# Kernel optimization log

Hardware: AMD Instinct MI355X
Metric: run time of the kernel (lower is better)

Reference implementation:

```python
import jax, jax.numpy as jnp
import numpy as np

N, E, IN, H, OUT, G = 40000, 640000, 128, 128, 16, 64


def _sage(x, src, dst, Wl, Wr, b, n):
    # PyG SAGEConv (aggr='mean'): out = lin_l(mean_j x_j) + lin_r(x_i); bias in lin_l only
    msg = jnp.take(x, src, axis=0)                      # [E, d] gather
    s = jax.ops.segment_sum(msg, dst, num_segments=n)   # [N, d] scatter-add
    cnt = jax.ops.segment_sum(jnp.ones((src.shape[0], 1), x.dtype), dst, num_segments=n)
    agg = s / jnp.maximum(cnt, 1.0)                     # mean; 0 for isolated nodes
    return agg @ Wl.T + x @ Wr.T + b


def setup_inputs() -> dict:
    key = jax.random.key(0)
    ks = jax.random.split(key, 12)
    x = jax.random.normal(ks[0], (N, IN), jnp.float32)
    edge_index = jax.random.randint(ks[1], (2, E), 0, N, jnp.int64)
    batch = jnp.sort(jax.random.randint(ks[2], (N,), 0, G, jnp.int64))
    def lin(k, o, i):
        return jax.random.normal(k, (o, i), jnp.float32) / np.sqrt(i)
    return {
        "x": x, "edge_index": edge_index, "batch": batch,
        "W1l": lin(ks[3], H, IN), "W1r": lin(ks[4], H, IN), "b1": jnp.zeros((H,), jnp.float32),
        "W2l": lin(ks[5], H, H),  "W2r": lin(ks[6], H, H),  "b2": jnp.zeros((H,), jnp.float32),
        "W3l": lin(ks[7], H, H),  "W3r": lin(ks[8], H, H),  "b3": jnp.zeros((H,), jnp.float32),
        "Wfc": lin(ks[9], OUT, H), "bfc": jnp.zeros((OUT,), jnp.float32),
    }


def reference(x, edge_index, batch, W1l, W1r, b1, W2l, W2r, b2, W3l, W3r, b3, Wfc, bfc):
    src, dst = edge_index[0], edge_index[1]
    n = x.shape[0]
    h = jax.nn.relu(_sage(x, src, dst, W1l, W1r, b1, n))
    h = jax.nn.relu(_sage(h, src, dst, W2l, W2r, b2, n))
    h = jax.nn.relu(_sage(h, src, dst, W3l, W3r, b3, n))
    # global_mean_pool over graph ids
    s = jax.ops.segment_sum(h, batch, num_segments=G)
    cnt = jax.ops.segment_sum(jnp.ones((n, 1), h.dtype), batch, num_segments=G)
    pooled = s / jnp.maximum(cnt, 1.0)                  # [G, H]
    return pooled @ Wfc.T + bfc                          # [G, OUT]
```

## Files before the change

### kernel.cpp

```cpp
#include <hip/hip_runtime.h>

static constexpr int D = 128;
static constexpr int PS = 32;

typedef __attribute__((ext_vector_type(8))) short short8;
typedef __attribute__((ext_vector_type(4))) float f32x4;

__device__ inline ushort f2bf(float f) {
  union { float f; unsigned u; } v; v.f = f;
  unsigned r = v.u + 0x7FFF + ((v.u >> 16) & 1);
  return (ushort)(r >> 16);
}
__device__ inline float bf2f_lo(unsigned p) {
  union { unsigned u; float f; } v; v.u = p << 16; return v.f;
}
__device__ inline float bf2f_hi(unsigned p) {
  union { unsigned u; float f; } v; v.u = p & 0xFFFF0000u; return v.f;
}

struct WPtrs { const float* s[6]; ushort* d[6]; };

__global__ __launch_bounds__(256) void k_prep(const float* __restrict__ x, ushort* __restrict__ xb, WPtrs p,
                                              const int* __restrict__ dst, int* __restrict__ hist,
                                              int n4x, int E) {
  int b = blockIdx.x, tid = threadIdx.x;
  int nxb = (n4x + 255) / 256;
  if (b < nxb) {
    int i = b * 256 + tid;
    if (i < n4x) {
      float4 v = *(const float4*)&x[i * 4];
      ushort4 o;
      o.x = f2bf(v.x); o.y = f2bf(v.y); o.z = f2bf(v.z); o.w = f2bf(v.w);
      *(ushort4*)&xb[i * 4] = o;
    }
  } else if (b < nxb + 96) {
    int idx = (b - nxb) * 256 + tid;
    int mat = idx >> 12;
    int off = (idx & 4095) * 4;
    float4 v = *(const float4*)&p.s[mat][off];
    ushort4 o;
    o.x = f2bf(v.x); o.y = f2bf(v.y); o.z = f2bf(v.z); o.w = f2bf(v.w);
    *(ushort4*)&p.d[mat][off] = o;
  } else {
    int e = (b - nxb - 96) * 256 + tid;
    if (e < E) atomicAdd(&hist[dst[e]], 1);
  }
}

__global__ __launch_bounds__(1024) void k_scan(const int* __restrict__ hist, int* __restrict__ offsets, int n) {
  __shared__ int wsum[16];
  int tid = threadIdx.x, lane = tid & 63, w = tid >> 6;
  int carry = 0;
  for (int base = 0; base < n; base += 8192) {
    int i0 = base + tid * 8;
    int v[8];
    #pragma unroll
    for (int j = 0; j < 8; ++j) { int i = i0 + j; v[j] = (i < n) ? hist[i] : 0; }
    int s = 0;
    #pragma unroll
    for (int j = 0; j < 8; ++j) { int t = v[j]; v[j] = s; s += t; }
    int x = s;
    #pragma unroll
    for (int off = 1; off < 64; off <<= 1) {
      int t = __shfl_up(x, off);
      if (lane >= off) x += t;
    }
    if (lane == 63) wsum[w] = x;
    __syncthreads();
    int wpre = 0, total = 0;
    #pragma unroll
    for (int k = 0; k < 16; ++k) { int t = wsum[k]; total += t; if (k < w) wpre += t; }
    int pre = carry + wpre + x - s;
    #pragma unroll
    for (int j = 0; j < 8; ++j) { int i = i0 + j; if (i < n) offsets[i] = pre + v[j]; }
    carry += total;
    __syncthreads();
  }
  if (tid == 0) offsets[n] = carry;
}

__global__ __launch_bounds__(256) void k_fill(const int* __restrict__ src, const int* __restrict__ dst,
                                              const int* __restrict__ offsets, int* __restrict__ cursor,
                                              int* __restrict__ ssrc, int E) {
  int e = blockIdx.x * 256 + threadIdx.x;
  if (e < E) {
    int d = dst[e];
    int pos = offsets[d] + atomicAdd(&cursor[d], 1);
    ssrc[pos] = src[e];
  }
}

__global__ __launch_bounds__(256) void k_layer(const ushort* __restrict__ Xin,
                                               const int* __restrict__ offsets, const int* __restrict__ ssrc,
                                               const ushort* __restrict__ Wl, const ushort* __restrict__ Wr,
                                               const float* __restrict__ bias, ushort* __restrict__ Out, int n) {
  __shared__ ushort atile[64][136];
  int tid = threadIdx.x;
  int wave = tid >> 6, lane = tid & 63;
  int q = lane >> 4, r = lane & 15;
  int base = blockIdx.x * 64;

  for (int i = 0; i < 16; ++i) {
    int node = base + wave * 16 + i;
    float acc[8];
    #pragma unroll
    for (int t = 0; t < 8; ++t) acc[t] = 0.f;
    int deg = 0;
    if (node < n) {
      int o0 = offsets[node];
      deg = offsets[node + 1] - o0;
      for (int c0 = 0; c0 < deg; c0 += 64) {
        int cn = min(64, deg - c0);
        int myid = (lane < cn) ? ssrc[o0 + c0 + lane] : 0;
        for (int j = 0; j < cn; j += 16) {
          uint4 buf[4];
          #pragma unroll
          for (int t = 0; t < 4; ++t) {
            int e = j + t * 4 + q;
            buf[t] = (uint4){0u, 0u, 0u, 0u};
            if (e < cn) {
              int s = __shfl(myid, e);
              buf[t] = *(const uint4*)&Xin[(size_t)s * D + r * 8];
            }
          }
          #pragma unroll
          for (int t = 0; t < 4; ++t) {
            acc[0] += bf2f_lo(buf[t].x); acc[1] += bf2f_hi(buf[t].x);
            acc[2] += bf2f_lo(buf[t].y); acc[3] += bf2f_hi(buf[t].y);
            acc[4] += bf2f_lo(buf[t].z); acc[5] += bf2f_hi(buf[t].z);
            acc[6] += bf2f_lo(buf[t].w); acc[7] += bf2f_hi(buf[t].w);
          }
        }
      }
    }
    #pragma unroll
    for (int t = 0; t < 8; ++t) {
      acc[t] += __shfl_xor(acc[t], 16);
      acc[t] += __shfl_xor(acc[t], 32);
    }
    if (q == 0) {
      float inv = 1.f / (float)max(deg, 1);
      uint4 o;
      o.x = (unsigned)f2bf(acc[0] * inv) | ((unsigned)f2bf(acc[1] * inv) << 16);
      o.y = (unsigned)f2bf(acc[2] * inv) | ((unsigned)f2bf(acc[3] * inv) << 16);
      o.z = (unsigned)f2bf(acc[4] * inv) | ((unsigned)f2bf(acc[5] * inv) << 16);
      o.w = (unsigned)f2bf(acc[6] * inv) | ((unsigned)f2bf(acc[7] * inv) << 16);
      *(uint4*)&atile[wave * 16 + i][r * 8] = o;
    }
  }
  __syncthreads();

  int wm = wave >> 1, wn = wave & 1;
  int m_base = base + wm * 32;
  int n_base = wn * 64;
  int kg = lane >> 4;

  f32x4 acc[2][4];
  #pragma unroll
  for (int i = 0; i < 2; ++i)
    #pragma unroll
    for (int j = 0; j < 4; ++j) acc[i][j] = (f32x4){0.f, 0.f, 0.f, 0.f};

  #pragma unroll
  for (int k0 = 0; k0 < 128; k0 += 32) {
    int kk = k0 + kg * 8;
    short8 a0[2], a1[2], b0[4], b1[4];
    #pragma unroll
    for (int fm = 0; fm < 2; ++fm) {
      a0[fm] = *(const short8*)&atile[wm * 32 + fm * 16 + r][kk];
      a1[fm] = *(const short8*)&Xin[(size_t)(m_base + fm * 16 + r) * D + kk];
    }
    #pragma unroll
    for (int fn = 0; fn < 4; ++fn) {
      b0[fn] = *(const short8*)&Wl[(size_t)(n_base + fn * 16 + r) * D + kk];
      b1[fn] = *(const short8*)&Wr[(size_t)(n_base + fn * 16 + r) * D + kk];
    }
    #pragma unroll
    for (int fm = 0; fm < 2; ++fm)
      #pragma unroll
      for (int fn = 0; fn < 4; ++fn) {
        acc[fm][fn] = __builtin_amdgcn_mfma_f32_16x16x32_bf16(a0[fm], b0[fn], acc[fm][fn], 0, 0, 0);
        acc[fm][fn] = __builtin_amdgcn_mfma_f32_16x16x32_bf16(a1[fm], b1[fn], acc[fm][fn], 0, 0, 0);
      }
  }
  #pragma unroll
  for (int fn = 0; fn < 4; ++fn) {
    int j = n_base + fn * 16 + r;
    float bj = bias[j];
    #pragma unroll
    for (int fm = 0; fm < 2; ++fm) {
      #pragma unroll
      for (int p = 0; p < 4; ++p) {
        int node = m_base + fm * 16 + kg * 4 + p;
        if (node < n) {
          float v = fmaxf(acc[fm][fn][p] + bj, 0.f);
          Out[(size_t)node * D + j] = f2bf(v);
        }
      }
    }
  }
}

__global__ __launch_bounds__(256) void k_pool_partial(const ushort* __restrict__ H, const int* __restrict__ batch,
                                                      float* __restrict__ partial, int n) {
  __shared__ float wsums[4][128];
  int g = blockIdx.x / PS, s = blockIdx.x % PS;
  int tid = threadIdx.x, wave = tid >> 6, lane = tid & 63;
  int a = 0, b = n;
  while (a < b) { int m = (a + b) >> 1; if (batch[m] < g) a = m + 1; else b = m; }
  int lo = a;
  b = n;
  while (a < b) { int m = (a + b) >> 1; if (batch[m] < g + 1) a = m + 1; else b = m; }
  int hi = a;
  int len = hi - lo;
  int chunk = (len + PS - 1) / PS;
  int a0 = lo + s * chunk;
  int a1 = min(a0 + chunk, hi);
  float ax = 0.f, ay = 0.f;
  for (int node = a0 + wave; node < a1; node += 4) {
    unsigned v = *(const unsigned*)&H[(size_t)node * D + lane * 2];
    ax += bf2f_lo(v);
    ay += bf2f_hi(v);
  }
  wsums[wave][lane * 2] = ax;
  wsums[wave][lane * 2 + 1] = ay;
  __syncthreads();
  if (tid < 128) {
    float v = wsums[0][tid] + wsums[1][tid] + wsums[2][tid] + wsums[3][tid];
    partial[(size_t)blockIdx.x * 128 + tid] = v;
  }
}

__global__ __launch_bounds__(256) void k_pool_fc2(const float* __restrict__ partial, const int* __restrict__ batch,
                                                  const float* __restrict__ Wfc, const float* __restrict__ bfc,
                                                  float* __restrict__ out, int n, int OUT) {
  __shared__ float pooled[128];
  int g = blockIdx.x;
  int tid = threadIdx.x, lane = tid & 63;
  int a = 0, b = n;
  while (a < b) { int m = (a + b) >> 1; if (batch[m] < g) a = m + 1; else b = m; }
  int lo = a;
  b = n;
  while (a < b) { int m = (a + b) >> 1; if (batch[m] < g + 1) a = m + 1; else b = m; }
  int hi = a;
  float inv = 1.f / (float)max(hi - lo, 1);
  if (tid < 128) {
    float v = 0.f;
    #pragma unroll
    for (int s = 0; s < PS; ++s) v += partial[(size_t)(g * PS + s) * 128 + tid];
    pooled[tid] = v * inv;
  }
  __syncthreads();
  if (tid < 64) {
    float2 p = *(const float2*)&pooled[lane * 2];
    for (int o = 0; o < OUT; ++o) {
      float2 w = *(const float2*)&Wfc[o * D + lane * 2];
      float part = p.x * w.x + p.y * w.y;
      #pragma unroll
      for (int off = 32; off > 0; off >>= 1) part += __shfl_down(part, off);
      if (lane == 0) out[g * OUT + o] = part + bfc[o];
    }
  }
}

extern "C" void kernel_launch(void* const* d_in, const int* in_sizes, int n_in,
                              void* d_out, int out_size, void* d_ws, size_t ws_size,
                              hipStream_t stream) {
  const float* x   = (const float*)d_in[0];
  const int* ei    = (const int*)d_in[1];
  const int* batch = (const int*)d_in[2];
  const float* W1l = (const float*)d_in[3];
  const float* W1r = (const float*)d_in[4];
  const float* b1  = (const float*)d_in[5];
  const float* W2l = (const float*)d_in[6];
  const float* W2r = (const float*)d_in[7];
  const float* b2  = (const float*)d_in[8];
  const float* W3l = (const float*)d_in[9];
  const float* W3r = (const float*)d_in[10];
  const float* b3  = (const float*)d_in[11];
  const float* Wfc = (const float*)d_in[12];
  const float* bfc = (const float*)d_in[13];
  float* out = (float*)d_out;

  int N = in_sizes[0] / D;
  int E = in_sizes[1] / 2;
  int OUT = in_sizes[12] / D;
  int G = out_size / OUT;
  const int* src = ei;
  const int* dst = ei + E;

  ushort* xb  = (ushort*)d_ws;
  ushort* h1  = xb + (size_t)N * D;
  ushort* h2  = h1 + (size_t)N * D;
  ushort* wb  = h2 + (size_t)N * D;
  int* ssrc   = (int*)(wb + 6 * 128 * 128);
  int* hist   = ssrc + E;
  int* cursor = hist + N;
  int* offsets = cursor + N;
  float* partial = (float*)(offsets + N + 2);

  ushort* wl1 = wb + 0 * 16384; ushort* wr1 = wb + 1 * 16384;
  ushort* wl2 = wb + 2 * 16384; ushort* wr2 = wb + 3 * 16384;
  ushort* wl3 = wb + 4 * 16384; ushort* wr3 = wb + 5 * 16384;

  hipMemsetAsync(hist, 0, (size_t)2 * N * 4, stream);

  WPtrs wp;
  wp.s[0] = W1l; wp.s[1] = W1r; wp.s[2] = W2l; wp.s[3] = W2r; wp.s[4] = W3l; wp.s[5] = W3r;
  wp.d[0] = wl1; wp.d[1] = wr1; wp.d[2] = wl2; wp.d[3] = wr2; wp.d[4] = wl3; wp.d[5] = wr3;

  int n4 = N * D / 4;
  int nxb = (n4 + 255) / 256;
  int eb = (E + 255) / 256;
  k_prep<<<nxb + 96 + eb, 256, 0, stream>>>(x, xb, wp, dst, hist, n4, E);
  k_scan<<<1, 1024, 0, stream>>>(hist, offsets, N);
  k_fill<<<eb, 256, 0, stream>>>(src, dst, offsets, cursor, ssrc, E);

  int gb = (N + 63) / 64;
  k_layer<<<gb, 256, 0, stream>>>(xb, offsets, ssrc, wl1, wr1, b1, h1, N);
  k_layer<<<gb, 256, 0, stream>>>(h1, offsets, ssrc, wl2, wr2, b2, h2, N);
  k_layer<<<gb, 256, 0, stream>>>(h2, offsets, ssrc, wl3, wr3, b3, h1, N);

  k_pool_partial<<<G * PS, 256, 0, stream>>>(h1, batch, partial, N);
  k_pool_fc2<<<G, 256, 0, stream>>>(partial, batch, Wfc, bfc, out, N, OUT);
}
```

Measured before the change: 321.3 us.

## Shrink layer tile to 16 nodes per block and replace memset with zero kernel

The fused SAGE layer kernel now handles 16 nodes per block instead of 64. Each wave aggregates 4 nodes and then computes a 16x32 output slice with MFMA, running the Wl pass and the Wr pass back to back. This gives four times as many blocks, spreading the irregular gather work more evenly across CUs and cutting per-block serial aggregation length, at the cost of more redundant weight loads per output. The hipMemsetAsync that cleared the histogram is replaced by a small zeroing kernel, meant to avoid memset launch overhead.

```diff
diff --git a/kernel.cpp b/kernel.cpp
--- a/kernel.cpp
+++ b/kernel.cpp
@@ -19,6 +19,11 @@
 }
 
 struct WPtrs { const float* s[6]; ushort* d[6]; };
+
+__global__ __launch_bounds__(256) void k_zero(uint4* __restrict__ p, int n16) {
+  int i = blockIdx.x * 256 + threadIdx.x;
+  if (i < n16) p[i] = (uint4){0u, 0u, 0u, 0u};
+}
 
 __global__ __launch_bounds__(256) void k_prep(const float* __restrict__ x, ushort* __restrict__ xb, WPtrs p,
                                               const int* __restrict__ dst, int* __restrict__ hist,
@@ -90,18 +95,19 @@
   }
 }
 
-__global__ __launch_bounds__(256) void k_layer(const ushort* __restrict__ Xin,
-                                               const int* __restrict__ offsets, const int* __restrict__ ssrc,
-                                               const ushort* __restrict__ Wl, const ushort* __restrict__ Wr,
-                                               const float* __restrict__ bias, ushort* __restrict__ Out, int n) {
-  __shared__ ushort atile[64][136];
+__global__ __launch_bounds__(256) void k_layer2(const ushort* __restrict__ Xin,
+                                                const int* __restrict__ offsets, const int* __restrict__ ssrc,
+                                                const ushort* __restrict__ Wl, const ushort* __restrict__ Wr,
+                                                const float* __restrict__ bias, ushort* __restrict__ Out, int n) {
+  __shared__ ushort atile[16][136];
   int tid = threadIdx.x;
   int wave = tid >> 6, lane = tid & 63;
   int q = lane >> 4, r = lane & 15;
-  int base = blockIdx.x * 64;
-
-  for (int i = 0; i < 16; ++i) {
-    int node = base + wave * 16 + i;
+  int base = blockIdx.x * 16;
+
+  for (int i = 0; i < 4; ++i) {
+    int row = wave * 4 + i;
+    int node = base + row;
     float acc[8];
     #pragma unroll
     for (int t = 0; t < 8; ++t) acc[t] = 0.f;
@@ -145,57 +151,45 @@
       o.y = (unsigned)f2bf(acc[2] * inv) | ((unsigned)f2bf(acc[3] * inv) << 16);
       o.z = (unsigned)f2bf(acc[4] * inv) | ((unsigned)f2bf(acc[5] * inv) << 16);
       o.w = (unsigned)f2bf(acc[6] * inv) | ((unsigned)f2bf(acc[7] * inv) << 16);
-      *(uint4*)&atile[wave * 16 + i][r * 8] = o;
+      *(uint4*)&atile[row][r * 8] = o;
     }
   }
   __syncthreads();
 
-  int wm = wave >> 1, wn = wave & 1;
-  int m_base = base + wm * 32;
-  int n_base = wn * 64;
+  int n_base = wave * 32;
   int kg = lane >> 4;
-
-  f32x4 acc[2][4];
-  #pragma unroll
-  for (int i = 0; i < 2; ++i)
-    #pragma unroll
-    for (int j = 0; j < 4; ++j) acc[i][j] = (f32x4){0.f, 0.f, 0.f, 0.f};
+  f32x4 acc2[2];
+  acc2[0] = (f32x4){0.f, 0.f, 0.f, 0.f};
+  acc2[1] = (f32x4){0.f, 0.f, 0.f, 0.f};
 
   #pragma unroll
   for (int k0 = 0; k0 < 128; k0 += 32) {
     int kk = k0 + kg * 8;
-    short8 a0[2], a1[2], b0[4], b1[4];
-    #pragma unroll
-    for (int fm = 0; fm < 2; ++fm) {
-      a0[fm] = *(const short8*)&atile[wm * 32 + fm * 16 + r][kk];
-      a1[fm] = *(const short8*)&Xin[(size_t)(m_base + fm * 16 + r) * D + kk];
-    }
-    #pragma unroll
-    for (int fn = 0; fn < 4; ++fn) {
-      b0[fn] = *(const short8*)&Wl[(size_t)(n_base + fn * 16 + r) * D + kk];
-      b1[fn] = *(const short8*)&Wr[(size_t)(n_base + fn * 16 + r) * D + kk];
-    }
-    #pragma unroll
-    for (int fm = 0; fm < 2; ++fm)
-      #pragma unroll
-      for (int fn = 0; fn < 4; ++fn) {
-        acc[fm][fn] = __builtin_amdgcn_mfma_f32_16x16x32_bf16(a0[fm], b0[fn], acc[fm][fn], 0, 0, 0);
-        acc[fm][fn] = __builtin_amdgcn_mfma_f32_16x16x32_bf16(a1[fm], b1[fn], acc[fm][fn], 0, 0, 0);
-      }
+    short8 a = *(const short8*)&atile[r][kk];
+    short8 b0 = *(const short8*)&Wl[(size_t)(n_base + r) * D + kk];
+    short8 b1 = *(const short8*)&Wl[(size_t)(n_base + 16 + r) * D + kk];
+    acc2[0] = __builtin_amdgcn_mfma_f32_16x16x32_bf16(a, b0, acc2[0], 0, 0, 0);
+    acc2[1] = __builtin_amdgcn_mfma_f32_16x16x32_bf16(a, b1, acc2[1], 0, 0, 0);
   }
   #pragma unroll
-  for (int fn = 0; fn < 4; ++fn) {
+  for (int k0 = 0; k0 < 128; k0 += 32) {
+    int kk = k0 + kg * 8;
+    short8 a = *(const short8*)&Xin[(size_t)(base + r) * D + kk];
+    short8 b0 = *(const short8*)&Wr[(size_t)(n_base + r) * D + kk];
+    short8 b1 = *(const short8*)&Wr[(size_t)(n_base + 16 + r) * D + kk];
+    acc2[0] = __builtin_amdgcn_mfma_f32_16x16x32_bf16(a, b0, acc2[0], 0, 0, 0);
+    acc2[1] = __builtin_amdgcn_mfma_f32_16x16x32_bf16(a, b1, acc2[1], 0, 0, 0);
+  }
+  #pragma unroll
+  for (int fn = 0; fn < 2; ++fn) {
     int j = n_base + fn * 16 + r;
     float bj = bias[j];
     #pragma unroll
-    for (int fm = 0; fm < 2; ++fm) {
-      #pragma unroll
-      for (int p = 0; p < 4; ++p) {
-        int node = m_base + fm * 16 + kg * 4 + p;
-        if (node < n) {
-          float v = fmaxf(acc[fm][fn][p] + bj, 0.f);
-          Out[(size_t)node * D + j] = f2bf(v);
-        }
+    for (int p = 0; p < 4; ++p) {
+      int node = base + kg * 4 + p;
+      if (node < n) {
+        float v = fmaxf(acc2[fn][p] + bj, 0.f);
+        Out[(size_t)node * D + j] = f2bf(v);
       }
     }
   }
@@ -303,11 +297,12 @@
   ushort* wl2 = wb + 2 * 16384; ushort* wr2 = wb + 3 * 16384;
   ushort* wl3 = wb + 4 * 16384; ushort* wr3 = wb + 5 * 16384;
 
-  hipMemsetAsync(hist, 0, (size_t)2 * N * 4, stream);
-
   WPtrs wp;
   wp.s[0] = W1l; wp.s[1] = W1r; wp.s[2] = W2l; wp.s[3] = W2r; wp.s[4] = W3l; wp.s[5] = W3r;
   wp.d[0] = wl1; wp.d[1] = wr1; wp.d[2] = wl2; wp.d[3] = wr2; wp.d[4] = wl3; wp.d[5] = wr3;
+
+  int n16 = (2 * N * 4) / 16;
+  k_zero<<<(n16 + 255) / 256, 256, 0, stream>>>((uint4*)hist, n16);
 
   int n4 = N * D / 4;
   int nxb = (n4 + 255) / 256;
@@ -316,10 +311,10 @@
   k_scan<<<1, 1024, 0, stream>>>(hist, offsets, N);
   k_fill<<<eb, 256, 0, stream>>>(src, dst, offsets, cursor, ssrc, E);
 
-  int gb = (N + 63) / 64;
-  k_layer<<<gb, 256, 0, stream>>>(xb, offsets, ssrc, wl1, wr1, b1, h1, N);
-  k_layer<<<gb, 256, 0, stream>>>(h1, offsets, ssrc, wl2, wr2, b2, h2, N);
-  k_layer<<<gb, 256, 0, stream>>>(h2, offsets, ssrc, wl3, wr3, b3, h1, N);
+  int lb = (N + 15) / 16;
+  k_layer2<<<lb, 256, 0, stream>>>(xb, offsets, ssrc, wl1, wr1, b1, h1, N);
+  k_layer2<<<lb, 256, 0, stream>>>(h1, offsets, ssrc, wl2, wr2, b2, h2, N);
+  k_layer2<<<lb, 256, 0, stream>>>(h2, offsets, ssrc, wl3, wr3, b3, h1, N);
 
   k_pool_partial<<<G * PS, 256, 0, stream>>>(h1, batch, partial, N);
   k_pool_fc2<<<G, 256, 0, stream>>>(partial, batch, Wfc, bfc, out, N, OUT);
```

Result: faster. 290.3 us (-9.7%).
